# Optimization experiments

Hardware: AMD Instinct MI355X
Metric: run time of the kernel (lower is better)

## Reference

```python
import jax, jax.numpy as jnp
import numpy as np

D_MODEL = 512
NUM_HEADS = 8
D_HEAD = D_MODEL // NUM_HEADS
D_FF = 2048
NUM_BUCKETS = 32
MAX_DISTANCE = 128
BATCH = 4
SEQ = 2048
LN_EPS = 1e-6


def _relative_position_bucket(relative_position, num_buckets, max_distance):
    # Bidirectional T5 bucketing (matches RelativePositionBias._relative_position_bucket).
    num_buckets = num_buckets // 2
    n = relative_position
    ret = (n < 0).astype(jnp.int32) * num_buckets
    n = jnp.abs(n)
    max_exact = num_buckets // 2
    is_small = n < max_exact
    val_if_large = max_exact + (
        jnp.log(n.astype(jnp.float32) / max_exact)
        / jnp.log(max_distance / max_exact)
        * (num_buckets - max_exact)
    ).astype(jnp.int32)
    val_if_large = jnp.minimum(val_if_large, num_buckets - 1)
    return ret + jnp.where(is_small, n, val_if_large)


def _layernorm(x, scale, bias):
    mu = jnp.mean(x, axis=-1, keepdims=True)
    var = jnp.mean(jnp.square(x - mu), axis=-1, keepdims=True)
    return (x - mu) * jax.lax.rsqrt(var + LN_EPS) * scale + bias


def setup_inputs() -> dict:
    key = jax.random.key(0)
    ks = jax.random.split(key, 16)
    w = 0.02  # weight init scale
    inp = {
        "x": jax.random.normal(ks[0], (BATCH, SEQ, D_MODEL), jnp.float32),
        "Wq": jax.random.normal(ks[1], (D_MODEL, D_MODEL), jnp.float32) * w,
        "bq": jnp.zeros((D_MODEL,), jnp.float32),
        "Wk": jax.random.normal(ks[2], (D_MODEL, D_MODEL), jnp.float32) * w,
        "bk": jnp.zeros((D_MODEL,), jnp.float32),
        "Wv": jax.random.normal(ks[3], (D_MODEL, D_MODEL), jnp.float32) * w,
        "bv": jnp.zeros((D_MODEL,), jnp.float32),
        "Wo": jax.random.normal(ks[4], (D_MODEL, D_MODEL), jnp.float32) * w,
        "bo": jnp.zeros((D_MODEL,), jnp.float32),
        "rel_bias": jax.random.normal(ks[5], (NUM_HEADS, NUM_BUCKETS), jnp.float32),
        "W1": jax.random.normal(ks[6], (D_MODEL, D_FF), jnp.float32) * w,
        "b1": jnp.zeros((D_FF,), jnp.float32),
        "W2": jax.random.normal(ks[7], (D_FF, D_MODEL), jnp.float32) * w,
        "b2": jnp.zeros((D_MODEL,), jnp.float32),
        "ln1_scale": jnp.ones((D_MODEL,), jnp.float32),
        "ln1_bias": jnp.zeros((D_MODEL,), jnp.float32),
        "ln2_scale": jnp.ones((D_MODEL,), jnp.float32),
        "ln2_bias": jnp.zeros((D_MODEL,), jnp.float32),
    }
    return inp


def _encoder_layer(x, Wq, bq, Wk, bk, Wv, bv, Wo, bo, rel_bias,
                   W1, b1, W2, b2, ln1_scale, ln1_bias, ln2_scale, ln2_bias):
    B, S, D = x.shape
    # QKV projections -> (B, H, S, Dh)
    def heads(t):
        return t.reshape(B, S, NUM_HEADS, D_HEAD).transpose(0, 2, 1, 3)
    q = heads(x @ Wq + bq)
    k = heads(x @ Wk + bk)
    v = heads(x @ Wv + bv)
    # Raw scores, then T5 relative-position bias, then scale (faithful order).
    scores = jnp.einsum("bhqd,bhkd->bhqk", q, k)
    pos = jnp.arange(S, dtype=jnp.int32)
    rel = pos[:, None] - pos[None, :]                           # (S, S)
    bucket = _relative_position_bucket(rel, NUM_BUCKETS, MAX_DISTANCE)
    bias = rel_bias[:, bucket]                                  # (H, S, S)
    scores = (scores + bias[None]) / jnp.sqrt(jnp.float32(D_HEAD))
    attn = jax.nn.softmax(scores, axis=-1)
    ctx = jnp.einsum("bhqk,bhkd->bhqd", attn, v)
    ctx = ctx.transpose(0, 2, 1, 3).reshape(B, S, D)
    attn_out = ctx @ Wo + bo
    # Residual + LayerNorm (post-LN), dropout inactive at eval.
    x = _layernorm(x + attn_out, ln1_scale, ln1_bias)
    # FFN: Linear -> ReLU -> Linear, residual + LayerNorm.
    ffn = jax.nn.relu(x @ W1 + b1) @ W2 + b2
    return _layernorm(x + ffn, ln2_scale, ln2_bias)


def reference(x, Wq, bq, Wk, bk, Wv, bv, Wo, bo, rel_bias,
              W1, b1, W2, b2, ln1_scale, ln1_bias, ln2_scale, ln2_bias):
    return _encoder_layer(x, Wq, bq, Wk, bk, Wv, bv, Wo, bo, rel_bias,
                          W1, b1, W2, b2, ln1_scale, ln1_bias, ln2_scale, ln2_bias)
```

## Files before the change

### kernel.cpp

```cpp
#include <hip/hip_runtime.h>

typedef __bf16 bf16_t;
typedef __bf16 bf16x8 __attribute__((ext_vector_type(8)));
typedef __bf16 bf16x4 __attribute__((ext_vector_type(4)));
typedef float  f32x4  __attribute__((ext_vector_type(4)));

#define MFMA_BF16 __builtin_amdgcn_mfma_f32_16x16x32_bf16

template <int N> __device__ __forceinline__ void wait_vmcnt() {
  if constexpr (N == 0)      asm volatile("s_waitcnt vmcnt(0)" ::: "memory");
  else if constexpr (N == 2) asm volatile("s_waitcnt vmcnt(2)" ::: "memory");
  else if constexpr (N == 4) asm volatile("s_waitcnt vmcnt(4)" ::: "memory");
  else if constexpr (N == 6) asm volatile("s_waitcnt vmcnt(6)" ::: "memory");
  else if constexpr (N == 8) asm volatile("s_waitcnt vmcnt(8)" ::: "memory");
}

__device__ __forceinline__ void gload_lds16(const void* g, void* l) {
  __builtin_amdgcn_global_load_lds((const __attribute__((address_space(1))) void*)g,
                                   (__attribute__((address_space(3))) void*)l,
                                   16, 0, 0);
}

__device__ __forceinline__ bf16x8 lds_frag(const bf16_t* base, int row, int c2) {
  return *(const bf16x8*)((const char*)base + ((((row) << 7) + c2) ^ ((row & 7) << 4)));
}

__global__ __launch_bounds__(256) void prep_k(const float* __restrict__ x, bf16_t* __restrict__ xb,
                                              const float* __restrict__ Wq, const float* __restrict__ Wk,
                                              const float* __restrict__ Wv, const float* __restrict__ Wo,
                                              const float* __restrict__ W1, const float* __restrict__ W2,
                                              bf16_t* __restrict__ WqkT, bf16_t* __restrict__ WvT,
                                              bf16_t* __restrict__ WoT, bf16_t* __restrict__ W1T,
                                              bf16_t* __restrict__ W2T,
                                              const float* __restrict__ relb, float* __restrict__ btab,
                                              const float* __restrict__ bq, const float* __restrict__ bk,
                                              float* __restrict__ bqk) {
  __shared__ float tsh[64][65];
  const int bid = blockIdx.x, tid = threadIdx.x;
  if (bid < 4096) {
    int i = bid * 256 + tid;
    float4 v = ((const float4*)x)[i];
    bf16x4 o = { (bf16_t)v.x, (bf16_t)v.y, (bf16_t)v.z, (bf16_t)v.w };
    ((bf16x4*)xb)[i] = o;
  } else if (bid < 4864) {
    int jid = bid - 4096;
    const float* src; bf16_t* dst; int K, N, n0, k0;
    if (jid < 256) {
      int wsel = jid >> 6, t = jid & 63;
      src = wsel == 0 ? Wq : wsel == 1 ? Wk : wsel == 2 ? Wv : Wo;
      dst = wsel == 0 ? WqkT : wsel == 1 ? (WqkT + 512 * 512) : wsel == 2 ? WvT : WoT;
      K = 512; N = 512; n0 = (t >> 3) * 64; k0 = (t & 7) * 64;
    } else if (jid < 512) {
      int t = jid - 256; src = W1; dst = W1T; K = 512; N = 2048;
      n0 = (t >> 3) * 64; k0 = (t & 7) * 64;
    } else {
      int t = jid - 512; src = W2; dst = W2T; K = 2048; N = 512;
      n0 = (t & 7) * 64; k0 = (t >> 3) * 64;
    }
    int tx = tid & 63, g = tid >> 6;
#pragma unroll
    for (int i = g; i < 64; i += 4) tsh[i][tx] = src[(size_t)(k0 + i) * N + n0 + tx];
    __syncthreads();
#pragma unroll
    for (int i = g; i < 64; i += 4)
      dst[(size_t)(n0 + i) * K + k0 + tx] = (bf16_t)tsh[tx][i];
  } else if (bid < 4992) {
    const float SCL = 0.125f * 1.44269504088896f;
    int i = (bid - 4864) * 256 + tid;
    if (i < 8 * 4095) {
      int h = i / 4095;
      int r = (i % 4095) - 2047;
      int ret = (r < 0) ? 16 : 0;
      int n = (r < 0) ? -r : r;
      int b;
      if (n < 8) b = n;
      else {
        float v = logf((float)n / 8.0f) / logf(16.0f) * 8.0f;
        int vi = 8 + (int)v;
        b = vi < 15 ? vi : 15;
      }
      btab[i] = relb[h * 32 + ret + b] * SCL;
    }
  } else {
    int i = (bid - 4992) * 256 + tid;
    if (i < 1024) bqk[i] = (i < 512) ? bq[i] : bk[i - 512];
  }
}

template <int BM, int BN, int WR, int WC, int NXB, int OUT_F32, int RELU, int BIASROW, int DBUF>
__global__ __launch_bounds__(WR * WC * 64) void gemm_k(const bf16_t* __restrict__ A,
                                                       const bf16_t* __restrict__ Bt,
                                                       const float* __restrict__ bias,
                                                       void* __restrict__ outp,
                                                       int M, int N, int K) {
  constexpr int NW = WR * WC;
  constexpr int AI = BM / WR / 16;
  constexpr int BJ = BN / WC / 16;
  constexpr int LPA = BM / (NW * 8);
  constexpr int LPB = BN / (NW * 8);
  constexpr int LPS = LPA + LPB;
  constexpr int MCH = NXB / 8;
  __shared__ __align__(16) bf16_t As[(DBUF + 1) * BM * 64];
  __shared__ __align__(16) bf16_t Bs[(DBUF + 1) * BN * 64];
  const int tid = threadIdx.x;
  const int lane = tid & 63, wid = tid >> 6;
  const int bid = blockIdx.x;
  const int xcd = bid & 7, li = bid >> 3;
  const int m0 = (xcd * MCH + li % MCH) * BM;
  const int n0 = (li / MCH) * BN;
  const int wr = wid / WC, wc = wid % WC;
  const int l15 = lane & 15, lg = lane >> 4;
  const int srow = lane >> 3;
  const int scolx = ((lane & 7) ^ srow) * 8;

  f32x4 acc[AI][BJ];
#pragma unroll
  for (int i = 0; i < AI; i++)
#pragma unroll
    for (int j = 0; j < BJ; j++) acc[i][j] = f32x4{0.f, 0.f, 0.f, 0.f};

  const bf16_t* Ag = A + (size_t)(m0 + wid * (BM / NW) + srow) * K + scolx;
  const bf16_t* Bg = Bt + (size_t)(n0 + wid * (BN / NW) + srow) * K + scolx;

  auto STG = [&](int buf, int k0) {
#pragma unroll
    for (int i = 0; i < LPA; i++)
      gload_lds16(Ag + (size_t)i * 8 * K + k0,
                  As + buf * (BM * 64) + wid * (BM / NW) * 64 + i * 8 * 64);
#pragma unroll
    for (int i = 0; i < LPB; i++)
      gload_lds16(Bg + (size_t)i * 8 * K + k0,
                  Bs + buf * (BN * 64) + wid * (BN / NW) * 64 + i * 8 * 64);
  };

  auto CMP = [&](int buf) {
    const bf16_t* AsB = As + buf * (BM * 64);
    const bf16_t* BsB = Bs + buf * (BN * 64);
#pragma unroll
    for (int ks = 0; ks < 2; ks++) {
      const int c2 = ks * 64 + lg * 16;
      bf16x8 af[AI], bfv[BJ];
#pragma unroll
      for (int i = 0; i < AI; i++)
        af[i] = lds_frag(AsB, wr * (BM / WR) + i * 16 + l15, c2);
#pragma unroll
      for (int j = 0; j < BJ; j++)
        bfv[j] = lds_frag(BsB, wc * (BN / WC) + j * 16 + l15, c2);
#pragma unroll
      for (int i = 0; i < AI; i++)
#pragma unroll
        for (int j = 0; j < BJ; j++)
          acc[i][j] = MFMA_BF16(af[i], bfv[j], acc[i][j], 0, 0, 0);
    }
  };

  if constexpr (DBUF) {
    STG(0, 0);
    const int NK = K >> 6;
#pragma unroll 2
    for (int t = 0; t < NK; t++) {
      const int buf = t & 1;
      __syncthreads();
      if (t + 1 < NK) {
        STG(buf ^ 1, (t + 1) << 6);
        wait_vmcnt<LPS>();
      } else {
        wait_vmcnt<0>();
      }
      CMP(buf);
    }
  } else {
    for (int k0 = 0; k0 < K; k0 += 64) {
      __syncthreads();
      STG(0, k0);
      wait_vmcnt<0>();
      __syncthreads();
      CMP(0);
    }
  }

  const int r0 = m0 + wr * (BM / WR) + (lg << 2);
  const int c0 = n0 + wc * (BN / WC) + l15;
#pragma unroll
  for (int j = 0; j < BJ; j++) {
    const int col = c0 + j * 16;
    const float bvc = BIASROW ? 0.f : bias[col];
#pragma unroll
    for (int i = 0; i < AI; i++) {
      const int row = r0 + i * 16;
#pragma unroll
      for (int r = 0; r < 4; r++) {
        float v = acc[i][j][r] + (BIASROW ? bias[row + r] : bvc);
        if (RELU) v = fmaxf(v, 0.f);
        if (OUT_F32) ((float*)outp)[(size_t)(row + r) * N + col] = v;
        else         ((bf16_t*)outp)[(size_t)(row + r) * N + col] = (bf16_t)v;
      }
    }
  }
}

__global__ __launch_bounds__(512) void attn_k(const bf16_t* __restrict__ Q,
                                              const bf16_t* __restrict__ Kp,
                                              const bf16_t* __restrict__ Vt,
                                              const float* __restrict__ btabS,
                                              const float* __restrict__ relb,
                                              bf16_t* __restrict__ ctx) {
  __shared__ __align__(16) bf16_t Ks[3][64 * 64];
  __shared__ __align__(16) bf16_t Vs[3][64 * 64];
  __shared__ __align__(16) bf16_t Ps[8][16 * 64];
  const int tid = threadIdx.x;
  const int lane = tid & 63, wid = tid >> 6;
  const int bid = blockIdx.x;
  const int xcd = bid & 7, tt = bid >> 3;
  const int qb = tt & 15, bh = (tt >> 4) * 8 + xcd;
  const int q0 = qb * 128;
  const int bb = bh >> 3, h = bh & 7;
  const size_t qkbase = (size_t)bb * 2048 * 1024;
  const size_t cbase = (size_t)bb * 2048 * 512;
  const int hc = h * 64;
  const int l15 = lane & 15, lg = lane >> 4;
  const int srow = lane >> 3;
  const int scolx = ((lane & 7) ^ srow) * 8;

  const bf16_t* qp = Q + qkbase + (size_t)(q0 + wid * 16 + l15) * 1024 + hc + lg * 8;
  bf16x8 qf0 = *(const bf16x8*)qp;
  bf16x8 qf1 = *(const bf16x8*)(qp + 32);

  const float SCL = 0.125f * 1.44269504088896f;
  const float* bt = btabS + (size_t)h * 4095 + 2047;
  const float cbp = relb[h * 32 + 15] * SCL;
  const float cbn = relb[h * 32 + 31] * SCL;

  float lrow = 0.f;
  f32x4 acc[4];
#pragma unroll
  for (int dn = 0; dn < 4; dn++) acc[dn] = f32x4{0.f, 0.f, 0.f, 0.f};
  char* pw = (char*)&Ps[wid][0];
  const int rq = q0 + wid * 16 + l15;

  const bf16_t* kg = Kp + qkbase + (size_t)(wid * 8 + srow) * 1024 + hc + scolx;
  const bf16_t* vg = Vt + (size_t)(hc + wid * 8 + srow) * 8192 + bb * 2048 + scolx;

#define STAGE(bufp, kv0)                                              \
  do {                                                                \
    gload_lds16(kg + (size_t)(kv0) * 1024, &Ks[bufp][wid * 8 * 64]);  \
    gload_lds16(vg + (kv0), &Vs[bufp][wid * 8 * 64]);                 \
  } while (0)

  auto TILE = [&](int t, int buf) {
    const int kv0 = t * 64;
    const bf16_t* KsB = &Ks[buf][0];
    const bf16_t* VsB = &Vs[buf][0];

    f32x4 s[4];
#pragma unroll
    for (int n = 0; n < 4; n++) s[n] = f32x4{0.f, 0.f, 0.f, 0.f};
    __builtin_amdgcn_s_setprio(1);
#pragma unroll
    for (int ks = 0; ks < 2; ks++) {
      bf16x8 qf = ks ? qf1 : qf0;
      const int c2 = ks * 64 + lg * 16;
#pragma unroll
      for (int n = 0; n < 4; n++) {
        bf16x8 kf = lds_frag(KsB, n * 16 + l15, c2);
        s[n] = MFMA_BF16(kf, qf, s[n], 0, 0, 0);
      }
    }
    __builtin_amdgcn_s_setprio(0);

    float lg2[4][4];
    const bool farp = (q0 - kv0) >= 192;
    const bool farn = (kv0 - q0) >= 256;
    if (farp || farn) {
      const float cb = farp ? cbp : cbn;
#pragma unroll
      for (int n = 0; n < 4; n++)
#pragma unroll
        for (int r = 0; r < 4; r++) lg2[n][r] = s[n][r] * SCL + cb;
    } else {
#pragma unroll
      for (int n = 0; n < 4; n++) {
        const float* btn = bt + (rq - kv0 - n * 16 - lg * 4);
#pragma unroll
        for (int r = 0; r < 4; r++) lg2[n][r] = s[n][r] * SCL + btn[-r];
      }
    }

#pragma unroll
    for (int n = 0; n < 4; n++) {
      float p0 = __builtin_amdgcn_exp2f(lg2[n][0]);
      float p1 = __builtin_amdgcn_exp2f(lg2[n][1]);
      float p2 = __builtin_amdgcn_exp2f(lg2[n][2]);
      float p3 = __builtin_amdgcn_exp2f(lg2[n][3]);
      lrow += (p0 + p1) + (p2 + p3);
      unsigned w0, w1;
      asm("v_cvt_pk_bf16_f32 %0, %1, %2" : "=v"(w0) : "v"(p0), "v"(p1));
      asm("v_cvt_pk_bf16_f32 %0, %1, %2" : "=v"(w1) : "v"(p2), "v"(p3));
      uint2 wv = {w0, w1};
      *(uint2*)(pw + (((l15 << 7) + n * 32 + (lg >> 1) * 16 + (lg & 1) * 8)
                      ^ ((l15 & 7) << 4))) = wv;
    }

    asm volatile("s_waitcnt lgkmcnt(0)" ::: "memory");
    __builtin_amdgcn_sched_barrier(0);

    __builtin_amdgcn_s_setprio(1);
#pragma unroll
    for (int ks = 0; ks < 2; ks++) {
      const int c2 = ks * 64 + lg * 16;
      bf16x8 pa = *(const bf16x8*)(pw + (((l15 << 7) + ks * 64 + (lg >> 1) * 32 + (lg & 1) * 16)
                                         ^ ((l15 & 7) << 4)));
#pragma unroll
      for (int dn = 0; dn < 4; dn++) {
        bf16x8 vf = lds_frag(VsB, dn * 16 + l15, c2);
        acc[dn] = MFMA_BF16(pa, vf, acc[dn], 0, 0, 0);
      }
    }
    __builtin_amdgcn_s_setprio(0);
  };

  STAGE(0, 0);
  STAGE(1, 64);

  int cur = 0, nx2 = 2;
  for (int t = 0; t < 31; t++) {
    wait_vmcnt<2>();
    __syncthreads();
    TILE(t, cur);
    if (t < 30) STAGE(nx2, (t + 2) * 64);
    cur = (cur == 2) ? 0 : cur + 1;
    nx2 = (nx2 == 2) ? 0 : nx2 + 1;
  }
  wait_vmcnt<0>();
  __syncthreads();
  TILE(31, cur);
#undef STAGE

  lrow += __shfl_xor(lrow, 16, 64);
  lrow += __shfl_xor(lrow, 32, 64);

  float li0 = __shfl(lrow, (lg << 2) + 0, 64);
  float li1 = __shfl(lrow, (lg << 2) + 1, 64);
  float li2 = __shfl(lrow, (lg << 2) + 2, 64);
  float li3 = __shfl(lrow, (lg << 2) + 3, 64);
  float inv[4] = {1.f / li0, 1.f / li1, 1.f / li2, 1.f / li3};
  const int qr0 = q0 + wid * 16 + (lg << 2);
#pragma unroll
  for (int dn = 0; dn < 4; dn++)
#pragma unroll
    for (int r = 0; r < 4; r++)
      ctx[cbase + (size_t)(qr0 + r) * 512 + hc + dn * 16 + l15] = (bf16_t)(acc[dn][r] * inv[r]);
}

__global__ __launch_bounds__(256) void lnres_k(const bf16_t* __restrict__ a,
                                               const bf16_t* __restrict__ bsrc,
                                               const float* __restrict__ sc,
                                               const float* __restrict__ bi,
                                               float* __restrict__ outf,
                                               bf16_t* __restrict__ outb) {
  int row = blockIdx.x * 4 + (threadIdx.x >> 6);
  int lane = threadIdx.x & 63;
  size_t base = (size_t)row * 512 + lane * 8;
  bf16x8 av8 = *(const bf16x8*)(a + base);
  bf16x8 bv8 = *(const bf16x8*)(bsrc + base);
  float v[8];
#pragma unroll
  for (int j = 0; j < 8; j++) v[j] = (float)av8[j] + (float)bv8[j];
  float s1 = 0.f, s2 = 0.f;
#pragma unroll
  for (int j = 0; j < 8; j++) { s1 += v[j]; s2 += v[j] * v[j]; }
#pragma unroll
  for (int off = 1; off < 64; off <<= 1) {
    s1 += __shfl_xor(s1, off, 64);
    s2 += __shfl_xor(s2, off, 64);
  }
  float mu = s1 * (1.f / 512.f);
  float var = s2 * (1.f / 512.f) - mu * mu;
  float rstd = rsqrtf(var + 1e-6f);
  int c = lane * 8;
  float4 sc0 = *(const float4*)(sc + c), sc1 = *(const float4*)(sc + c + 4);
  float4 bi0 = *(const float4*)(bi + c), bi1 = *(const float4*)(bi + c + 4);
  float scv[8] = {sc0.x, sc0.y, sc0.z, sc0.w, sc1.x, sc1.y, sc1.z, sc1.w};
  float biv[8] = {bi0.x, bi0.y, bi0.z, bi0.w, bi1.x, bi1.y, bi1.z, bi1.w};
  float o[8];
#pragma unroll
  for (int j = 0; j < 8; j++) o[j] = (v[j] - mu) * rstd * scv[j] + biv[j];
  if (outf) {
    *(float4*)(outf + base) = make_float4(o[0], o[1], o[2], o[3]);
    *(float4*)(outf + base + 4) = make_float4(o[4], o[5], o[6], o[7]);
  }
  if (outb) {
    bf16x8 ob = {(bf16_t)o[0], (bf16_t)o[1], (bf16_t)o[2], (bf16_t)o[3],
                 (bf16_t)o[4], (bf16_t)o[5], (bf16_t)o[6], (bf16_t)o[7]};
    *(bf16x8*)(outb + base) = ob;
  }
}

extern "C" void kernel_launch(void* const* d_in, const int* in_sizes, int n_in,
                              void* d_out, int out_size, void* d_ws, size_t ws_size,
                              hipStream_t stream) {
  const float* x    = (const float*)d_in[0];
  const float* Wq   = (const float*)d_in[1];
  const float* bq   = (const float*)d_in[2];
  const float* Wk   = (const float*)d_in[3];
  const float* bk   = (const float*)d_in[4];
  const float* Wv   = (const float*)d_in[5];
  const float* bv   = (const float*)d_in[6];
  const float* Wo   = (const float*)d_in[7];
  const float* bo   = (const float*)d_in[8];
  const float* relb = (const float*)d_in[9];
  const float* W1   = (const float*)d_in[10];
  const float* b1   = (const float*)d_in[11];
  const float* W2   = (const float*)d_in[12];
  const float* b2   = (const float*)d_in[13];
  const float* ln1s = (const float*)d_in[14];
  const float* ln1b = (const float*)d_in[15];
  const float* ln2s = (const float*)d_in[16];
  const float* ln2b = (const float*)d_in[17];

  char* w = (char*)d_ws;
  bf16_t* xb    = (bf16_t*)(w + 0);
  bf16_t* qk    = (bf16_t*)(w + 8388608);
  bf16_t* tmpb  = (bf16_t*)(w + 8388608);
  bf16_t* vtg   = (bf16_t*)(w + 25165824);
  bf16_t* ctxb  = (bf16_t*)(w + 33554432);
  bf16_t* tmpb2 = (bf16_t*)(w + 33554432);
  bf16_t* x1b   = (bf16_t*)(w + 50331648);
  bf16_t* WqkT  = (bf16_t*)(w + 58720256);
  bf16_t* WvT   = (bf16_t*)(w + 59768832);
  bf16_t* WoT   = (bf16_t*)(w + 60293120);
  bf16_t* W1T   = (bf16_t*)(w + 60817408);
  bf16_t* W2T   = (bf16_t*)(w + 62914560);
  float*  btab  = (float*)(w + 65011712);
  float*  bqk   = (float*)(w + 65273856);
  bf16_t* ffh   = (bf16_t*)(w + 67108864);

  prep_k<<<4996, 256, 0, stream>>>(x, xb, Wq, Wk, Wv, Wo, W1, W2,
                                   WqkT, WvT, WoT, W1T, W2T,
                                   relb, btab, bq, bk, bqk);

  gemm_k<128, 128, 2, 2, 64, 0, 0, 0, 1><<<512, 256, 0, stream>>>(xb, WqkT, bqk, qk, 8192, 1024, 512);
  gemm_k<64, 128, 1, 4, 8, 0, 0, 1, 1><<<512, 256, 0, stream>>>(WvT, xb, bv, vtg, 512, 8192, 512);

  attn_k<<<512, 512, 0, stream>>>(qk, qk + 512, vtg, btab, relb, ctxb);

  gemm_k<64, 128, 1, 4, 128, 0, 0, 0, 1><<<512, 256, 0, stream>>>(ctxb, WoT, bo, tmpb, 8192, 512, 512);
  lnres_k<<<2048, 256, 0, stream>>>(xb, tmpb, ln1s, ln1b, (float*)nullptr, x1b);

  gemm_k<128, 128, 2, 2, 64, 0, 1, 0, 0><<<1024, 256, 0, stream>>>(x1b, W1T, b1, ffh, 8192, 2048, 512);
  gemm_k<64, 128, 1, 4, 128, 0, 0, 0, 1><<<512, 256, 0, stream>>>(ffh, W2T, b2, tmpb2, 8192, 512, 2048);
  lnres_k<<<2048, 256, 0, stream>>>(x1b, tmpb2, ln2s, ln2b, (float*)d_out, (bf16_t*)nullptr);
}
```

Measured before the change: 167.0 us.

## Give each attention wave two 16-row query groups to reuse K/V fragments

The attention kernel moves from 8 waves handling 16 query rows each to 4 waves handling 32 rows each, in two row groups per wave. Each K and V fragment read from LDS now feeds two MFMAs, which halves LDS fragment traffic per unit of work and gives more independent MFMAs to interleave. Staging issues four global-to-LDS loads per thread instead of two, and the wait count is adjusted to match. In exchange the kernel has fewer waves per block and more registers per wave, which may lower occupancy and latency hiding.

Measured after the change: 173.6 us. 1.04x slower.

```diff
diff --git a/kernel.cpp b/kernel.cpp
--- a/kernel.cpp
+++ b/kernel.cpp
@@ -199,7 +199,7 @@
   }
 }
 
-__global__ __launch_bounds__(512) void attn_k(const bf16_t* __restrict__ Q,
+__global__ __launch_bounds__(256) void attn_k(const bf16_t* __restrict__ Q,
                                               const bf16_t* __restrict__ Kp,
                                               const bf16_t* __restrict__ Vt,
                                               const float* __restrict__ btabS,
@@ -207,7 +207,7 @@
                                               bf16_t* __restrict__ ctx) {
   __shared__ __align__(16) bf16_t Ks[3][64 * 64];
   __shared__ __align__(16) bf16_t Vs[3][64 * 64];
-  __shared__ __align__(16) bf16_t Ps[8][16 * 64];
+  __shared__ __align__(16) bf16_t Ps[4][2][16 * 64];
   const int tid = threadIdx.x;
   const int lane = tid & 63, wid = tid >> 6;
   const int bid = blockIdx.x;
@@ -222,29 +222,39 @@
   const int srow = lane >> 3;
   const int scolx = ((lane & 7) ^ srow) * 8;
 
-  const bf16_t* qp = Q + qkbase + (size_t)(q0 + wid * 16 + l15) * 1024 + hc + lg * 8;
-  bf16x8 qf0 = *(const bf16x8*)qp;
-  bf16x8 qf1 = *(const bf16x8*)(qp + 32);
+  bf16x8 qf[2][2];
+#pragma unroll
+  for (int rg = 0; rg < 2; rg++) {
+    const bf16_t* qp = Q + qkbase + (size_t)(q0 + wid * 32 + rg * 16 + l15) * 1024 + hc + lg * 8;
+    qf[rg][0] = *(const bf16x8*)qp;
+    qf[rg][1] = *(const bf16x8*)(qp + 32);
+  }
 
   const float SCL = 0.125f * 1.44269504088896f;
   const float* bt = btabS + (size_t)h * 4095 + 2047;
   const float cbp = relb[h * 32 + 15] * SCL;
   const float cbn = relb[h * 32 + 31] * SCL;
 
-  float lrow = 0.f;
-  f32x4 acc[4];
-#pragma unroll
-  for (int dn = 0; dn < 4; dn++) acc[dn] = f32x4{0.f, 0.f, 0.f, 0.f};
-  char* pw = (char*)&Ps[wid][0];
-  const int rq = q0 + wid * 16 + l15;
-
-  const bf16_t* kg = Kp + qkbase + (size_t)(wid * 8 + srow) * 1024 + hc + scolx;
-  const bf16_t* vg = Vt + (size_t)(hc + wid * 8 + srow) * 8192 + bb * 2048 + scolx;
-
-#define STAGE(bufp, kv0)                                              \
-  do {                                                                \
-    gload_lds16(kg + (size_t)(kv0) * 1024, &Ks[bufp][wid * 8 * 64]);  \
-    gload_lds16(vg + (kv0), &Vs[bufp][wid * 8 * 64]);                 \
+  float lrow[2] = {0.f, 0.f};
+  f32x4 acc[2][4];
+#pragma unroll
+  for (int rg = 0; rg < 2; rg++)
+#pragma unroll
+    for (int dn = 0; dn < 4; dn++) acc[rg][dn] = f32x4{0.f, 0.f, 0.f, 0.f};
+  char* pw0 = (char*)&Ps[wid][0][0];
+  char* pw1 = (char*)&Ps[wid][1][0];
+  const int rq0 = q0 + wid * 32 + l15;
+  const int rq1 = rq0 + 16;
+
+  const bf16_t* kg = Kp + qkbase + (size_t)(wid * 16 + srow) * 1024 + hc + scolx;
+  const bf16_t* vg = Vt + (size_t)(hc + wid * 16 + srow) * 8192 + bb * 2048 + scolx;
+
+#define STAGE(bufp, kv0)                                                           \
+  do {                                                                             \
+    gload_lds16(kg + (size_t)(kv0) * 1024, &Ks[bufp][wid * 16 * 64]);              \
+    gload_lds16(kg + (size_t)((kv0) + 8) * 1024, &Ks[bufp][(wid * 16 + 8) * 64]);  \
+    gload_lds16(vg + (kv0), &Vs[bufp][wid * 16 * 64]);                             \
+    gload_lds16(vg + (kv0) + 8 * 8192, &Vs[bufp][(wid * 16 + 8) * 64]);            \
   } while (0)
 
   auto TILE = [&](int t, int buf) {
@@ -252,53 +262,59 @@
     const bf16_t* KsB = &Ks[buf][0];
     const bf16_t* VsB = &Vs[buf][0];
 
-    f32x4 s[4];
-#pragma unroll
-    for (int n = 0; n < 4; n++) s[n] = f32x4{0.f, 0.f, 0.f, 0.f};
+    f32x4 s[2][4];
+#pragma unroll
+    for (int rg = 0; rg < 2; rg++)
+#pragma unroll
+      for (int n = 0; n < 4; n++) s[rg][n] = f32x4{0.f, 0.f, 0.f, 0.f};
     __builtin_amdgcn_s_setprio(1);
 #pragma unroll
     for (int ks = 0; ks < 2; ks++) {
-      bf16x8 qf = ks ? qf1 : qf0;
       const int c2 = ks * 64 + lg * 16;
 #pragma unroll
       for (int n = 0; n < 4; n++) {
         bf16x8 kf = lds_frag(KsB, n * 16 + l15, c2);
-        s[n] = MFMA_BF16(kf, qf, s[n], 0, 0, 0);
+        s[0][n] = MFMA_BF16(kf, qf[0][ks], s[0][n], 0, 0, 0);
+        s[1][n] = MFMA_BF16(kf, qf[1][ks], s[1][n], 0, 0, 0);
       }
     }
     __builtin_amdgcn_s_setprio(0);
 
-    float lg2[4][4];
     const bool farp = (q0 - kv0) >= 192;
     const bool farn = (kv0 - q0) >= 256;
-    if (farp || farn) {
-      const float cb = farp ? cbp : cbn;
-#pragma unroll
-      for (int n = 0; n < 4; n++)
-#pragma unroll
-        for (int r = 0; r < 4; r++) lg2[n][r] = s[n][r] * SCL + cb;
-    } else {
+#pragma unroll
+    for (int rg = 0; rg < 2; rg++) {
+      const int rq = rg ? rq1 : rq0;
+      char* pw = rg ? pw1 : pw0;
+      float lg2[4][4];
+      if (farp || farn) {
+        const float cb = farp ? cbp : cbn;
+#pragma unroll
+        for (int n = 0; n < 4; n++)
+#pragma unroll
+          for (int r = 0; r < 4; r++) lg2[n][r] = s[rg][n][r] * SCL + cb;
+      } else {
+#pragma unroll
+        for (int n = 0; n < 4; n++) {
+          const float* btn = bt + (rq - kv0 - n * 16 - lg * 4);
+#pragma unroll
+          for (int r = 0; r < 4; r++) lg2[n][r] = s[rg][n][r] * SCL + btn[-r];
+        }
+      }
 #pragma unroll
       for (int n = 0; n < 4; n++) {
-        const float* btn = bt + (rq - kv0 - n * 16 - lg * 4);
-#pragma unroll
-        for (int r = 0; r < 4; r++) lg2[n][r] = s[n][r] * SCL + btn[-r];
-      }
-    }
-
-#pragma unroll
-    for (int n = 0; n < 4; n++) {
-      float p0 = __builtin_amdgcn_exp2f(lg2[n][0]);
-      float p1 = __builtin_amdgcn_exp2f(lg2[n][1]);
-      float p2 = __builtin_amdgcn_exp2f(lg2[n][2]);
-      float p3 = __builtin_amdgcn_exp2f(lg2[n][3]);
-      lrow += (p0 + p1) + (p2 + p3);
-      unsigned w0, w1;
-      asm("v_cvt_pk_bf16_f32 %0, %1, %2" : "=v"(w0) : "v"(p0), "v"(p1));
-      asm("v_cvt_pk_bf16_f32 %0, %1, %2" : "=v"(w1) : "v"(p2), "v"(p3));
-      uint2 wv = {w0, w1};
-      *(uint2*)(pw + (((l15 << 7) + n * 32 + (lg >> 1) * 16 + (lg & 1) * 8)
-                      ^ ((l15 & 7) << 4))) = wv;
+        float p0 = __builtin_amdgcn_exp2f(lg2[n][0]);
+        float p1 = __builtin_amdgcn_exp2f(lg2[n][1]);
+        float p2 = __builtin_amdgcn_exp2f(lg2[n][2]);
+        float p3 = __builtin_amdgcn_exp2f(lg2[n][3]);
+        lrow[rg] += (p0 + p1) + (p2 + p3);
+        unsigned w0, w1;
+        asm("v_cvt_pk_bf16_f32 %0, %1, %2" : "=v"(w0) : "v"(p0), "v"(p1));
+        asm("v_cvt_pk_bf16_f32 %0, %1, %2" : "=v"(w1) : "v"(p2), "v"(p3));
+        uint2 wv = {w0, w1};
+        *(uint2*)(pw + (((l15 << 7) + n * 32 + (lg >> 1) * 16 + (lg & 1) * 8)
+                        ^ ((l15 & 7) << 4))) = wv;
+      }
     }
 
     asm volatile("s_waitcnt lgkmcnt(0)" ::: "memory");
@@ -308,12 +324,14 @@
 #pragma unroll
     for (int ks = 0; ks < 2; ks++) {
       const int c2 = ks * 64 + lg * 16;
-      bf16x8 pa = *(const bf16x8*)(pw + (((l15 << 7) + ks * 64 + (lg >> 1) * 32 + (lg & 1) * 16)
-                                         ^ ((l15 & 7) << 4)));
+      const int po = ((l15 << 7) + ks * 64 + (lg >> 1) * 32 + (lg & 1) * 16) ^ ((l15 & 7) << 4);
+      bf16x8 pa0 = *(const bf16x8*)(pw0 + po);
+      bf16x8 pa1 = *(const bf16x8*)(pw1 + po);
 #pragma unroll
       for (int dn = 0; dn < 4; dn++) {
         bf16x8 vf = lds_frag(VsB, dn * 16 + l15, c2);
-        acc[dn] = MFMA_BF16(pa, vf, acc[dn], 0, 0, 0);
+        acc[0][dn] = MFMA_BF16(pa0, vf, acc[0][dn], 0, 0, 0);
+        acc[1][dn] = MFMA_BF16(pa1, vf, acc[1][dn], 0, 0, 0);
       }
     }
     __builtin_amdgcn_s_setprio(0);
@@ -324,7 +342,7 @@
 
   int cur = 0, nx2 = 2;
   for (int t = 0; t < 31; t++) {
-    wait_vmcnt<2>();
+    wait_vmcnt<4>();
     __syncthreads();
     TILE(t, cur);
     if (t < 30) STAGE(nx2, (t + 2) * 64);
@@ -336,20 +354,23 @@
   TILE(31, cur);
 #undef STAGE
 
-  lrow += __shfl_xor(lrow, 16, 64);
-  lrow += __shfl_xor(lrow, 32, 64);
-
-  float li0 = __shfl(lrow, (lg << 2) + 0, 64);
-  float li1 = __shfl(lrow, (lg << 2) + 1, 64);
-  float li2 = __shfl(lrow, (lg << 2) + 2, 64);
-  float li3 = __shfl(lrow, (lg << 2) + 3, 64);
-  float inv[4] = {1.f / li0, 1.f / li1, 1.f / li2, 1.f / li3};
-  const int qr0 = q0 + wid * 16 + (lg << 2);
-#pragma unroll
-  for (int dn = 0; dn < 4; dn++)
-#pragma unroll
-    for (int r = 0; r < 4; r++)
-      ctx[cbase + (size_t)(qr0 + r) * 512 + hc + dn * 16 + l15] = (bf16_t)(acc[dn][r] * inv[r]);
+#pragma unroll
+  for (int rg = 0; rg < 2; rg++) {
+    float lr = lrow[rg];
+    lr += __shfl_xor(lr, 16, 64);
+    lr += __shfl_xor(lr, 32, 64);
+    float li0 = __shfl(lr, (lg << 2) + 0, 64);
+    float li1 = __shfl(lr, (lg << 2) + 1, 64);
+    float li2 = __shfl(lr, (lg << 2) + 2, 64);
+    float li3 = __shfl(lr, (lg << 2) + 3, 64);
+    float inv[4] = {1.f / li0, 1.f / li1, 1.f / li2, 1.f / li3};
+    const int qr0 = q0 + wid * 32 + rg * 16 + (lg << 2);
+#pragma unroll
+    for (int dn = 0; dn < 4; dn++)
+#pragma unroll
+      for (int r = 0; r < 4; r++)
+        ctx[cbase + (size_t)(qr0 + r) * 512 + hc + dn * 16 + l15] = (bf16_t)(acc[rg][dn][r] * inv[r]);
+  }
 }
 
 __global__ __launch_bounds__(256) void lnres_k(const bf16_t* __restrict__ a,
@@ -442,7 +463,7 @@
   gemm_k<128, 128, 2, 2, 64, 0, 0, 0, 1><<<512, 256, 0, stream>>>(xb, WqkT, bqk, qk, 8192, 1024, 512);
   gemm_k<64, 128, 1, 4, 8, 0, 0, 1, 1><<<512, 256, 0, stream>>>(WvT, xb, bv, vtg, 512, 8192, 512);
 
-  attn_k<<<512, 512, 0, stream>>>(qk, qk + 512, vtg, btab, relb, ctxb);
+  attn_k<<<512, 256, 0, stream>>>(qk, qk + 512, vtg, btab, relb, ctxb);
 
   gemm_k<64, 128, 1, 4, 128, 0, 0, 0, 1><<<512, 256, 0, stream>>>(ctxb, WoT, bo, tmpb, 8192, 512, 512);
   lnres_k<<<2048, 256, 0, stream>>>(xb, tmpb, ln1s, ln1b, (float*)nullptr, x1b);
```
